# Performance work log

Hardware: AMD Instinct MI355X
Metric: run time of the kernel (lower is better)

## Reference

```python
import jax, jax.numpy as jnp
import numpy as np

B, T, D, H, K = 8, 4096, 768, 12, 64
EPS_WKV = 1e-9
EPS_GN = 1e-5


def setup_inputs() -> dict:
    key = jax.random.key(0)
    ks = jax.random.split(key, 12)
    x = jax.random.normal(ks[0], (B, T, D), jnp.float32)
    # linear projection weights (torch nn.Linear stores [out, in]; y = x @ W.T)
    W_r = jax.random.normal(ks[1], (D, D), jnp.float32) * 0.02
    W_k = jax.random.normal(ks[2], (D, D), jnp.float32) * 0.02
    W_v = jax.random.normal(ks[3], (D, D), jnp.float32) * 0.02
    W_o = jax.random.normal(ks[4], (D, D), jnp.float32) * 0.02
    time_mix_r = jax.random.uniform(ks[5], (D,), jnp.float32)
    time_mix_k = jax.random.uniform(ks[6], (D,), jnp.float32)
    time_mix_v = jax.random.uniform(ks[7], (D,), jnp.float32)
    # around the module's init values (time_decay ~ -0.075, time_first ~ 0.15 at layer 6/12)
    time_decay = -0.075 + 0.1 * jax.random.normal(ks[8], (H, K), jnp.float32)
    time_first = 0.15 + 0.1 * jax.random.normal(ks[9], (H, K), jnp.float32)
    gn_weight = jnp.ones((D,), jnp.float32)
    gn_bias = jnp.zeros((D,), jnp.float32)
    return {
        "x": x,
        "time_mix_r": time_mix_r, "time_mix_k": time_mix_k, "time_mix_v": time_mix_v,
        "time_decay": time_decay, "time_first": time_first,
        "W_r": W_r, "W_k": W_k, "W_v": W_v, "W_o": W_o,
        "gn_weight": gn_weight, "gn_bias": gn_bias,
    }


def reference(x, time_mix_r, time_mix_k, time_mix_v, time_decay, time_first,
              W_r, W_k, W_v, W_o, gn_weight, gn_bias):
    Bx, Tx, Dx = x.shape
    Hx, Kx = time_decay.shape
    # token-shift: previous timestep (zero-initialized state)
    x_prev = jnp.concatenate([jnp.zeros_like(x[:, :1]), x[:, :-1]], axis=1)
    xr = x * time_mix_r + x_prev * (1.0 - time_mix_r)
    xk = x * time_mix_k + x_prev * (1.0 - time_mix_k)
    xv = x * time_mix_v + x_prev * (1.0 - time_mix_v)
    r = jax.nn.sigmoid(xr @ W_r.T).reshape(Bx, Tx, Hx, Kx)
    k = (xk @ W_k.T).reshape(Bx, Tx, Hx, Kx)
    v = (xv @ W_v.T).reshape(Bx, Tx, Hx, Kx)

    w = jnp.exp(-jnp.exp(time_decay))   # [H,K] decay per channel
    eu = jnp.exp(time_first)            # [H,K] bonus for current token

    def step(carry, kv_t):
        num, den = carry                # each [B,H,K]
        k_t, v_t = kv_t                 # each [B,H,K]
        ek = jnp.exp(k_t)
        wkv = (num + eu * ek * v_t) / (den + eu * ek + EPS_WKV)
        return (num * w + ek * v_t, den * w + ek), wkv

    k_tm = jnp.moveaxis(k, 1, 0)        # [T,B,H,K]
    v_tm = jnp.moveaxis(v, 1, 0)
    init = (jnp.zeros((Bx, Hx, Kx), x.dtype), jnp.zeros((Bx, Hx, Kx), x.dtype))
    _, wkv = jax.lax.scan(step, init, (k_tm, v_tm))
    out = jnp.moveaxis(wkv, 0, 1)       # [B,T,H,K]

    y = r * out                         # [B,T,H,K]
    # torch GroupNorm(H, D) on [B, D, T]: normalize each group over (K channels x T steps)
    mean = y.mean(axis=(1, 3), keepdims=True)
    var = y.var(axis=(1, 3), keepdims=True)
    y = (y - mean) * jax.lax.rsqrt(var + EPS_GN)
    y = y * gn_weight.reshape(1, 1, Hx, Kx) + gn_bias.reshape(1, 1, Hx, Kx)
    return y.reshape(Bx, Tx, Dx) @ W_o.T
```

## Files before the change

### kernel.cpp

```cpp
#include <hip/hip_runtime.h>
#include <hip/hip_bf16.h>
#include <cstdint>

#define B_ 8
#define T_ 4096
#define D_ 768
#define H_ 12
#define M_ (B_*T_)
#define CHUNKS 256
#define CLEN 16
#define WELEM (D_*D_)
#define NCH (B_*H_*64)

typedef __attribute__((ext_vector_type(8))) short bf16x8;
typedef __attribute__((ext_vector_type(4))) float f32x4;

static __device__ __forceinline__ unsigned short f2bf(float f) {
  __hip_bfloat16 h = __float2bfloat16(f);
  return __builtin_bit_cast(unsigned short, h);
}
static __device__ __forceinline__ float bf2f(unsigned short u) {
  unsigned v = ((unsigned)u) << 16;
  return __builtin_bit_cast(float, v);
}

static __device__ __forceinline__ void async16(const void* g, void* l) {
  __builtin_amdgcn_global_load_lds(
      (const __attribute__((address_space(1))) unsigned int*)g,
      (__attribute__((address_space(3))) unsigned int*)l, 16, 0, 0);
}

__global__ __launch_bounds__(256) void zero_out_kernel(float* __restrict__ out, size_t n4) {
  size_t gid = (size_t)blockIdx.x * 256 + threadIdx.x;
  if (gid < n4) *(float4*)(out + gid * 4) = make_float4(0.f, 0.f, 0.f, 0.f);
}

__global__ __launch_bounds__(256) void mix_kernel(
    const float* __restrict__ x, const float* __restrict__ tmr,
    const float* __restrict__ tmk, const float* __restrict__ tmv,
    unsigned short* __restrict__ xr, unsigned short* __restrict__ xk,
    unsigned short* __restrict__ xv) {
  size_t gid = (size_t)blockIdx.x * 256 + threadIdx.x;
  size_t idx4 = gid * 4;
  int d = (int)(idx4 % D_);
  size_t row = idx4 / D_;
  int t = (int)(row & (T_ - 1));
  float4 xc = *(const float4*)(x + idx4);
  float4 xp = make_float4(0.f, 0.f, 0.f, 0.f);
  if (t > 0) xp = *(const float4*)(x + idx4 - D_);
  float4 mr = *(const float4*)(tmr + d);
  float4 mk = *(const float4*)(tmk + d);
  float4 mv = *(const float4*)(tmv + d);
  ushort4 orr, okk, ovv;
  orr.x = f2bf(xc.x*mr.x + xp.x*(1.f-mr.x));
  orr.y = f2bf(xc.y*mr.y + xp.y*(1.f-mr.y));
  orr.z = f2bf(xc.z*mr.z + xp.z*(1.f-mr.z));
  orr.w = f2bf(xc.w*mr.w + xp.w*(1.f-mr.w));
  okk.x = f2bf(xc.x*mk.x + xp.x*(1.f-mk.x));
  okk.y = f2bf(xc.y*mk.y + xp.y*(1.f-mk.y));
  okk.z = f2bf(xc.z*mk.z + xp.z*(1.f-mk.z));
  okk.w = f2bf(xc.w*mk.w + xp.w*(1.f-mk.w));
  ovv.x = f2bf(xc.x*mv.x + xp.x*(1.f-mv.x));
  ovv.y = f2bf(xc.y*mv.y + xp.y*(1.f-mv.y));
  ovv.z = f2bf(xc.z*mv.z + xp.z*(1.f-mv.z));
  ovv.w = f2bf(xc.w*mv.w + xp.w*(1.f-mv.w));
  *(ushort4*)(xr + idx4) = orr;
  *(ushort4*)(xk + idx4) = okk;
  *(ushort4*)(xv + idx4) = ovv;
}

__global__ __launch_bounds__(256) void wconv_kernel(
    const float* __restrict__ a, const float* __restrict__ b,
    const float* __restrict__ c, const float* __restrict__ d,
    unsigned short* __restrict__ o) {
  size_t gid = (size_t)blockIdx.x * 256 + threadIdx.x;
  size_t idx4 = gid * 4;
  size_t mi = idx4 / WELEM;
  size_t off = idx4 % WELEM;
  const float* src = (mi == 0) ? a : (mi == 1) ? b : (mi == 2) ? c : d;
  float4 v = *(const float4*)(src + off);
  ushort4 u;
  u.x = f2bf(v.x); u.y = f2bf(v.y); u.z = f2bf(v.z); u.w = f2bf(v.w);
  *(ushort4*)(o + idx4) = u;
}

template<int ACT, int OBF>
__global__ __launch_bounds__(256) void gemm_nt(
    const unsigned short* __restrict__ A,
    const unsigned short* __restrict__ Bw,
    void* __restrict__ Cv, int M, int N, int Kd) {
  __shared__ __align__(16) unsigned short smem[128 * 128];
  unsigned short* As = smem;
  unsigned short* Bs = smem + 128 * 64;
  const int tid = threadIdx.x;
  const int wave = tid >> 6, lane = tid & 63;
  const int quad = lane >> 4, l16 = lane & 15;

  int nwg = gridDim.x * gridDim.y;
  int lin = blockIdx.y * gridDim.x + blockIdx.x;
  int q = nwg >> 3, r = nwg & 7;
  int xcd = lin & 7, off = lin >> 3;
  int swz = (xcd < r ? xcd * (q + 1) : r * (q + 1) + (xcd - r) * q) + off;
  const int m0 = (swz / gridDim.x) * 128;
  const int n0 = (swz % gridDim.x) * 128;
  const int wm = (wave & 1) * 64, wn = (wave >> 1) * 64;

  f32x4 acc[4][4] = {};

  for (int kb = 0; kb < Kd; kb += 64) {
    __syncthreads();
#pragma unroll
    for (int j = 0; j < 4; ++j) {
      int chunk = j * 256 + tid;
      int row = chunk >> 3, slot = chunk & 7;
      int ks = slot ^ (row & 7);
      async16(A  + ((size_t)(m0 + row) * Kd + kb + ks * 8), &As[chunk * 8]);
      async16(Bw + ((size_t)(n0 + row) * Kd + kb + ks * 8), &Bs[chunk * 8]);
    }
    __syncthreads();

#pragma unroll
    for (int kk = 0; kk < 2; ++kk) {
      bf16x8 a[4], b[4];
#pragma unroll
      for (int i = 0; i < 4; ++i) {
        int ra = wm + i * 16 + l16;
        a[i] = *(const bf16x8*)&As[ra * 64 + (((kk * 4 + quad) ^ (ra & 7)) * 8)];
        int rb = wn + i * 16 + l16;
        b[i] = *(const bf16x8*)&Bs[rb * 64 + (((kk * 4 + quad) ^ (rb & 7)) * 8)];
      }
#pragma unroll
      for (int i = 0; i < 4; ++i)
#pragma unroll
        for (int jj = 0; jj < 4; ++jj)
          acc[i][jj] = __builtin_amdgcn_mfma_f32_16x16x32_bf16(a[i], b[jj], acc[i][jj], 0, 0, 0);
    }
  }

  if (OBF) {
    __syncthreads();
    unsigned short* Cs = smem;
#pragma unroll
    for (int i = 0; i < 4; ++i) {
#pragma unroll
      for (int jj = 0; jj < 4; ++jj) {
        int col = wn + jj * 16 + l16;
#pragma unroll
        for (int rr = 0; rr < 4; ++rr) {
          int row = wm + i * 16 + quad * 4 + rr;
          float v = acc[i][jj][rr];
          if (ACT == 1) v = 1.f / (1.f + __expf(-v));
          int cg = (col >> 3) ^ (row & 7);
          Cs[row * 128 + cg * 8 + (col & 7)] = f2bf(v);
        }
      }
    }
    __syncthreads();
#pragma unroll
    for (int g = 0; g < 8; ++g) {
      int gi = g * 256 + tid;
      int row = gi >> 4, cg = gi & 15;
      int sg = cg ^ (row & 7);
      bf16x8 vv = *(const bf16x8*)&Cs[row * 128 + sg * 8];
      *(bf16x8*)((unsigned short*)Cv + (size_t)(m0 + row) * N + n0 + cg * 8) = vv;
    }
  } else {
#pragma unroll
    for (int i = 0; i < 4; ++i) {
      int rowb = m0 + wm + i * 16 + quad * 4;
#pragma unroll
      for (int jj = 0; jj < 4; ++jj) {
        int col = n0 + wn + jj * 16 + l16;
#pragma unroll
        for (int rr = 0; rr < 4; ++rr) {
          float v = acc[i][jj][rr];
          ((float*)Cv)[(size_t)(rowb + rr) * N + col] = v;
        }
      }
    }
  }
}

__global__ __launch_bounds__(256) void wkv_pass1(
    const unsigned short* __restrict__ Kb, const unsigned short* __restrict__ Vb,
    const float* __restrict__ td,
    float* __restrict__ sumN, float* __restrict__ sumD) {
  int gid = blockIdx.x * 256 + threadIdx.x;
  int kg = gid & 7;
  int tmp = gid >> 3;
  int h = tmp % H_;
  tmp /= H_;
  int b = tmp % B_;
  int c = tmp / B_;
  const float* tdp = td + h * 64 + kg * 8;
  float w[8], num[8], den[8];
#pragma unroll
  for (int j = 0; j < 8; ++j) {
    w[j] = __expf(-__expf(tdp[j]));
    num[j] = 0.f; den[j] = 0.f;
  }
  size_t base = ((size_t)(b * T_ + c * CLEN)) * D_ + h * 64 + kg * 8;
#pragma unroll 4
  for (int i = 0; i < CLEN; ++i) {
    bf16x8 k8 = *(const bf16x8*)(Kb + base + (size_t)i * D_);
    bf16x8 v8 = *(const bf16x8*)(Vb + base + (size_t)i * D_);
#pragma unroll
    for (int j = 0; j < 8; ++j) {
      float ek = __expf(bf2f((unsigned short)k8[j]));
      num[j] = num[j] * w[j] + ek * bf2f((unsigned short)v8[j]);
      den[j] = den[j] * w[j] + ek;
    }
  }
  int ob = ((c * B_ + b) * H_ + h) * 64 + kg * 8;
  *(float4*)(sumN + ob)     = make_float4(num[0], num[1], num[2], num[3]);
  *(float4*)(sumN + ob + 4) = make_float4(num[4], num[5], num[6], num[7]);
  *(float4*)(sumD + ob)     = make_float4(den[0], den[1], den[2], den[3]);
  *(float4*)(sumD + ob + 4) = make_float4(den[4], den[5], den[6], den[7]);
}

__global__ __launch_bounds__(256) void wkv_pass2(
    const float* __restrict__ sumN, const float* __restrict__ sumD,
    const float* __restrict__ td,
    float* __restrict__ prefN, float* __restrict__ prefD,
    float* __restrict__ gstats) {
  int tid = blockIdx.x * 256 + threadIdx.x;
  if (blockIdx.x == 0 && threadIdx.x < 192) gstats[threadIdx.x] = 0.f;
  int k = tid & 63;
  int h = (tid >> 6) % H_;
  float w = __expf(-__expf(td[h * 64 + k]));
  float wL = w;
#pragma unroll
  for (int i = 0; i < 4; ++i) wL *= wL;
  float n = 0.f, d = 0.f;
  for (int c = 0; c < CHUNKS; ++c) {
    int j = c * NCH + tid;
    prefN[j] = n; prefD[j] = d;
    n = n * wL + sumN[j];
    d = d * wL + sumD[j];
  }
}

__global__ __launch_bounds__(256) void wkv_pass3(
    const unsigned short* __restrict__ Kb, const unsigned short* __restrict__ Vb,
    unsigned short* __restrict__ RY,
    const float* __restrict__ td, const float* __restrict__ tf,
    const float* __restrict__ prefN, const float* __restrict__ prefD,
    float* __restrict__ gsum, float* __restrict__ gsq) {
  int gid = blockIdx.x * 256 + threadIdx.x;
  int kg = gid & 7;
  int tmp = gid >> 3;
  int h = tmp % H_;
  tmp /= H_;
  int b = tmp % B_;
  int c = tmp / B_;
  const float* tdp = td + h * 64 + kg * 8;
  const float* tfp = tf + h * 64 + kg * 8;
  float w[8], eu[8], num[8], den[8];
  int sb = ((c * B_ + b) * H_ + h) * 64 + kg * 8;
  float4 n0 = *(const float4*)(prefN + sb), n1 = *(const float4*)(prefN + sb + 4);
  float4 d0 = *(const float4*)(prefD + sb), d1 = *(const float4*)(prefD + sb + 4);
  num[0]=n0.x; num[1]=n0.y; num[2]=n0.z; num[3]=n0.w;
  num[4]=n1.x; num[5]=n1.y; num[6]=n1.z; num[7]=n1.w;
  den[0]=d0.x; den[1]=d0.y; den[2]=d0.z; den[3]=d0.w;
  den[4]=d1.x; den[5]=d1.y; den[6]=d1.z; den[7]=d1.w;
#pragma unroll
  for (int j = 0; j < 8; ++j) {
    w[j]  = __expf(-__expf(tdp[j]));
    eu[j] = __expf(tfp[j]);
  }
  size_t base = ((size_t)(b * T_ + c * CLEN)) * D_ + h * 64 + kg * 8;
  float s1 = 0.f, s2 = 0.f;
#pragma unroll 4
  for (int i = 0; i < CLEN; ++i) {
    size_t idx = base + (size_t)i * D_;
    bf16x8 k8 = *(const bf16x8*)(Kb + idx);
    bf16x8 v8 = *(const bf16x8*)(Vb + idx);
    bf16x8 r8 = *(const bf16x8*)(RY + idx);
    bf16x8 y8;
#pragma unroll
    for (int j = 0; j < 8; ++j) {
      float kk = bf2f((unsigned short)k8[j]);
      float vv = bf2f((unsigned short)v8[j]);
      float rr = bf2f((unsigned short)r8[j]);
      float ek = __expf(kk);
      float wkv = (num[j] + eu[j] * ek * vv) / (den[j] + eu[j] * ek + 1e-9f);
      unsigned short ybf = f2bf(rr * wkv);
      y8[j] = (short)ybf;
      float y = bf2f(ybf);
      s1 += y; s2 += y * y;
      num[j] = num[j] * w[j] + ek * vv;
      den[j] = den[j] * w[j] + ek;
    }
    *(bf16x8*)(RY + idx) = y8;
  }
#pragma unroll
  for (int off = 4; off; off >>= 1) {
    s1 += __shfl_xor(s1, off);
    s2 += __shfl_xor(s2, off);
  }
  if (kg == 0) {
    atomicAdd(&gsum[b * H_ + h], s1);
    atomicAdd(&gsq [b * H_ + h], s2);
  }
}

__global__ __launch_bounds__(256) void gn_kernel(
    const unsigned short* __restrict__ Y, const float* __restrict__ gsum,
    const float* __restrict__ gsq, const float* __restrict__ gw,
    const float* __restrict__ gb, unsigned short* __restrict__ Ybf) {
  size_t gid = (size_t)blockIdx.x * 256 + threadIdx.x;
  size_t idx4 = gid * 4;
  int d = (int)(idx4 % D_);
  size_t row = idx4 / D_;
  int b = (int)(row >> 12);
  int h = d >> 6;
  int g = b * H_ + h;
  const float inv = 1.f / (float)(T_ * 64);
  float mean = gsum[g] * inv;
  float var = gsq[g] * inv - mean * mean;
  float rstd = rsqrtf(var + 1e-5f);
  ushort4 yu = *(const ushort4*)(Y + idx4);
  float4 wv = *(const float4*)(gw + d);
  float4 bv = *(const float4*)(gb + d);
  ushort4 o;
  o.x = f2bf((bf2f(yu.x) - mean) * rstd * wv.x + bv.x);
  o.y = f2bf((bf2f(yu.y) - mean) * rstd * wv.y + bv.y);
  o.z = f2bf((bf2f(yu.z) - mean) * rstd * wv.z + bv.z);
  o.w = f2bf((bf2f(yu.w) - mean) * rstd * wv.w + bv.w);
  *(ushort4*)(Ybf + idx4) = o;
}

extern "C" void kernel_launch(void* const* d_in, const int* in_sizes, int n_in,
                              void* d_out, int out_size, void* d_ws, size_t ws_size,
                              hipStream_t stream) {
  (void)in_sizes; (void)n_in;
  const float* x   = (const float*)d_in[0];
  const float* tmr = (const float*)d_in[1];
  const float* tmk = (const float*)d_in[2];
  const float* tmv = (const float*)d_in[3];
  const float* td  = (const float*)d_in[4];
  const float* tf  = (const float*)d_in[5];
  const float* Wr  = (const float*)d_in[6];
  const float* Wk  = (const float*)d_in[7];
  const float* Wv  = (const float*)d_in[8];
  const float* Wo  = (const float*)d_in[9];
  const float* gw  = (const float*)d_in[10];
  const float* gb  = (const float*)d_in[11];
  float* out = (float*)d_out;

  constexpr size_t MD = (size_t)M_ * D_;
  constexpr size_t NEED = 4 * (MD * 2)
                        + (size_t)4 * WELEM * 2
                        + 4 * ((size_t)CHUNKS * NCH * 4)
                        + 1024;
  if (ws_size < NEED) {
    zero_out_kernel<<<(int)((MD / 4 + 255) / 256), 256, 0, stream>>>(out, MD / 4);
    return;
  }

  char* ws = (char*)d_ws;
  unsigned short* XR = (unsigned short*)ws; ws += MD * 2;
  unsigned short* XK = (unsigned short*)ws; ws += MD * 2;
  unsigned short* XV = (unsigned short*)ws; ws += MD * 2;
  unsigned short* Rb = (unsigned short*)ws; ws += MD * 2;
  unsigned short* Wb = (unsigned short*)ws; ws += (size_t)4 * WELEM * 2;
  float* sumN  = (float*)ws; ws += (size_t)CHUNKS * NCH * 4;
  float* sumD  = (float*)ws; ws += (size_t)CHUNKS * NCH * 4;
  float* prefN = (float*)ws; ws += (size_t)CHUNKS * NCH * 4;
  float* prefD = (float*)ws; ws += (size_t)CHUNKS * NCH * 4;
  float* gstats = (float*)ws; ws += 1024;
  unsigned short* Kb = XR;
  unsigned short* Vb = XK;
  unsigned short* Yb = XV;

  mix_kernel<<<(int)(MD / 1024), 256, 0, stream>>>(x, tmr, tmk, tmv, XR, XK, XV);
  wconv_kernel<<<(4 * WELEM / 4) / 256, 256, 0, stream>>>(Wr, Wk, Wv, Wo, Wb);

  dim3 ggrid(D_ / 128, M_ / 128);
  gemm_nt<1, 1><<<ggrid, 256, 0, stream>>>(XR, Wb,             Rb, M_, D_, D_);
  gemm_nt<0, 1><<<ggrid, 256, 0, stream>>>(XK, Wb + WELEM,     Kb, M_, D_, D_);
  gemm_nt<0, 1><<<ggrid, 256, 0, stream>>>(XV, Wb + 2 * WELEM, Vb, M_, D_, D_);

  wkv_pass1<<<(CHUNKS * NCH / 8) / 256, 256, 0, stream>>>(Kb, Vb, td, sumN, sumD);
  wkv_pass2<<<NCH / 256, 256, 0, stream>>>(sumN, sumD, td, prefN, prefD, gstats);
  wkv_pass3<<<(CHUNKS * NCH / 8) / 256, 256, 0, stream>>>(Kb, Vb, Rb, td, tf,
                                                          prefN, prefD, gstats, gstats + 96);
  gn_kernel<<<(int)(MD / 1024), 256, 0, stream>>>(Rb, gstats, gstats + 96, gw, gb, Yb);

  gemm_nt<0, 0><<<ggrid, 256, 0, stream>>>(Yb, Wb + 3 * WELEM, out, M_, D_, D_);
}
```

Measured before the change: 538.3 us.

## Double-buffer GEMM shared tiles and parallelize chunk prefix scan

The GEMM kernel now uses two shared-memory tile buffers and issues the next K-tile's async loads before computing the current one, so global loads overlap the MFMA work. The WKV chunk-prefix pass becomes a per-channel block-wide Hillis–Steele scan over the 256 chunks instead of a serial loop per thread, greatly increasing parallelism. The per-element divide in pass3 uses a fast approximate divide. This doubles GEMM LDS usage, which may reduce occupancy; pass2 reads are now strided, and the fast divide slightly changes precision.

```diff
diff --git a/kernel.cpp b/kernel.cpp
--- a/kernel.cpp
+++ b/kernel.cpp
@@ -89,9 +89,7 @@
     const unsigned short* __restrict__ A,
     const unsigned short* __restrict__ Bw,
     void* __restrict__ Cv, int M, int N, int Kd) {
-  __shared__ __align__(16) unsigned short smem[128 * 128];
-  unsigned short* As = smem;
-  unsigned short* Bs = smem + 128 * 64;
+  __shared__ __align__(16) unsigned short smem[2][128 * 128];
   const int tid = threadIdx.x;
   const int wave = tid >> 6, lane = tid & 63;
   const int quad = lane >> 4, l16 = lane & 15;
@@ -105,10 +103,9 @@
   const int n0 = (swz % gridDim.x) * 128;
   const int wm = (wave & 1) * 64, wn = (wave >> 1) * 64;
 
-  f32x4 acc[4][4] = {};
-
-  for (int kb = 0; kb < Kd; kb += 64) {
-    __syncthreads();
+  auto stage = [&](int buf, int kb) {
+    unsigned short* As = smem[buf];
+    unsigned short* Bs = smem[buf] + 128 * 64;
 #pragma unroll
     for (int j = 0; j < 4; ++j) {
       int chunk = j * 256 + tid;
@@ -117,8 +114,17 @@
       async16(A  + ((size_t)(m0 + row) * Kd + kb + ks * 8), &As[chunk * 8]);
       async16(Bw + ((size_t)(n0 + row) * Kd + kb + ks * 8), &Bs[chunk * 8]);
     }
-    __syncthreads();
-
+  };
+
+  f32x4 acc[4][4] = {};
+
+  stage(0, 0);
+  __syncthreads();
+  int cur = 0;
+  for (int kb = 0; kb < Kd; kb += 64) {
+    if (kb + 64 < Kd) stage(cur ^ 1, kb + 64);
+    const unsigned short* As = smem[cur];
+    const unsigned short* Bs = smem[cur] + 128 * 64;
 #pragma unroll
     for (int kk = 0; kk < 2; ++kk) {
       bf16x8 a[4], b[4];
@@ -135,11 +141,12 @@
         for (int jj = 0; jj < 4; ++jj)
           acc[i][jj] = __builtin_amdgcn_mfma_f32_16x16x32_bf16(a[i], b[jj], acc[i][jj], 0, 0, 0);
     }
+    __syncthreads();
+    cur ^= 1;
   }
 
   if (OBF) {
-    __syncthreads();
-    unsigned short* Cs = smem;
+    unsigned short* Cs = smem[0];
 #pragma unroll
     for (int i = 0; i < 4; ++i) {
 #pragma unroll
@@ -223,21 +230,35 @@
     const float* __restrict__ td,
     float* __restrict__ prefN, float* __restrict__ prefD,
     float* __restrict__ gstats) {
-  int tid = blockIdx.x * 256 + threadIdx.x;
-  if (blockIdx.x == 0 && threadIdx.x < 192) gstats[threadIdx.x] = 0.f;
-  int k = tid & 63;
-  int h = (tid >> 6) % H_;
+  int ch = blockIdx.x;
+  int c = threadIdx.x;
+  if (ch == 0 && c < 192) gstats[c] = 0.f;
+  int k = ch & 63;
+  int h = (ch >> 6) % H_;
   float w = __expf(-__expf(td[h * 64 + k]));
   float wL = w;
 #pragma unroll
   for (int i = 0; i < 4; ++i) wL *= wL;
-  float n = 0.f, d = 0.f;
-  for (int c = 0; c < CHUNKS; ++c) {
-    int j = c * NCH + tid;
-    prefN[j] = n; prefD[j] = d;
-    n = n * wL + sumN[j];
-    d = d * wL + sumD[j];
-  }
+  __shared__ float Aa[256], Nn[256], Dd[256];
+  int j = c * NCH + ch;
+  float a = wL, n = sumN[j], d = sumD[j];
+  Aa[c] = a; Nn[c] = n; Dd[c] = d;
+  __syncthreads();
+  for (int off = 1; off < 256; off <<= 1) {
+    float aL = 0.f, nL = 0.f, dL = 0.f;
+    if (c >= off) { aL = Aa[c - off]; nL = Nn[c - off]; dL = Dd[c - off]; }
+    __syncthreads();
+    if (c >= off) {
+      n = nL * a + n;
+      d = dL * a + d;
+      a = aL * a;
+      Aa[c] = a; Nn[c] = n; Dd[c] = d;
+    }
+    __syncthreads();
+  }
+  float pn = 0.f, pd = 0.f;
+  if (c > 0) { pn = Nn[c - 1]; pd = Dd[c - 1]; }
+  prefN[j] = pn; prefD[j] = pd;
 }
 
 __global__ __launch_bounds__(256) void wkv_pass3(
@@ -283,7 +304,7 @@
       float vv = bf2f((unsigned short)v8[j]);
       float rr = bf2f((unsigned short)r8[j]);
       float ek = __expf(kk);
-      float wkv = (num[j] + eu[j] * ek * vv) / (den[j] + eu[j] * ek + 1e-9f);
+      float wkv = __fdividef(num[j] + eu[j] * ek * vv, den[j] + eu[j] * ek + 1e-9f);
       unsigned short ybf = f2bf(rr * wkv);
       y8[j] = (short)ybf;
       float y = bf2f(ybf);
@@ -382,7 +403,7 @@
   gemm_nt<0, 1><<<ggrid, 256, 0, stream>>>(XV, Wb + 2 * WELEM, Vb, M_, D_, D_);
 
   wkv_pass1<<<(CHUNKS * NCH / 8) / 256, 256, 0, stream>>>(Kb, Vb, td, sumN, sumD);
-  wkv_pass2<<<NCH / 256, 256, 0, stream>>>(sumN, sumD, td, prefN, prefD, gstats);
+  wkv_pass2<<<NCH, 256, 0, stream>>>(sumN, sumD, td, prefN, prefD, gstats);
   wkv_pass3<<<(CHUNKS * NCH / 8) / 256, 256, 0, stream>>>(Kb, Vb, Rb, td, tf,
                                                           prefN, prefD, gstats, gstats + 96);
   gn_kernel<<<(int)(MD / 1024), 256, 0, stream>>>(Rb, gstats, gstats + 96, gw, gb, Yb);
```

New measurement: 571.9 us. +6.3%, slower.
